# Performance work log

Measured on AMD Instinct MI355X. Metric: run time of the kernel, lower is better.

Reference implementation:

```python
import jax, jax.numpy as jnp
import numpy as np

# Dims: B INRs, N probe points, d_in=2 coords, hidden H, out D_OUT, proj P
B, N, D_IN, H, D_OUT, P = 128, 4096, 2, 128, 3, 128
W0_SIREN = 30.0  # SIREN frequency scale
LN_EPS = 1e-5


def setup_inputs() -> dict:
    key = jax.random.key(0)
    ks = jax.random.split(key, 12)
    sn = lambda k, shape, sc: (jax.random.normal(k, shape, dtype=jnp.float32) * sc)
    return {
        # per-sample SIREN params, torch layout: weight [b, in, out, 1], bias [b, out, 1]
        "w0": sn(ks[0], (B, D_IN, H, 1), 1.0 / D_IN),
        "w1": sn(ks[1], (B, H, H, 1), np.sqrt(6.0 / H) / W0_SIREN),
        "w2": sn(ks[2], (B, H, D_OUT, 1), np.sqrt(6.0 / H) / W0_SIREN),
        "b0": sn(ks[3], (B, H, 1), 0.1),
        "b1": sn(ks[4], (B, H, 1), 0.1),
        "b2": sn(ks[5], (B, D_OUT, 1), 0.1),
        # learned probe coordinates, initialized U[-1, 1) as in the module
        "inputs": jax.random.uniform(ks[6], (1, N, D_IN), dtype=jnp.float32, minval=-1.0, maxval=1.0),
        # projection (num_inputs -> proj_dim) + LayerNorm params, one per probed layer (4 total)
        "pw": sn(ks[7], (4, N, P), 1.0 / np.sqrt(N)),
        "pb": jnp.zeros((4, P), jnp.float32),
        "ln_g": jnp.ones((4, P), jnp.float32),
        "ln_b": jnp.zeros((4, P), jnp.float32),
    }


def _layernorm(x, g, b):
    m = jnp.mean(x, axis=-1, keepdims=True)
    v = jnp.mean(jnp.square(x - m), axis=-1, keepdims=True)
    return (x - m) * jax.lax.rsqrt(v + LN_EPS) * g + b


def reference(w0, w1, w2, b0, b1, b2, inputs, pw, pb, ln_g, ln_b):
    b = w0.shape[0]
    x = jnp.broadcast_to(inputs, (b,) + inputs.shape[1:])  # [b, n, d_in]

    def lin(h, W, bb):
        # per-sample linear: [b,n,i] @ [b,i,o] + [b,1,o]
        return jnp.einsum('bni,bio->bno', h, W[..., 0]) + bb[:, None, :, 0]

    h1 = jnp.sin(W0_SIREN * lin(x, w0, b0))   # [b, n, H]
    h2 = jnp.sin(W0_SIREN * lin(h1, w1, b1))  # [b, n, H]
    h3 = lin(h2, w2, b2)                      # [b, n, D_OUT] (last layer: no sine)
    feats = [x, h1, h2, h3]  # probe features per node layer (input coords + activations)

    outs = []
    for i, f in enumerate(feats):
        # permute to [b, dim_i, n], project n -> P, then LayerNorm over P
        z = jnp.einsum('bnd,np->bdp', f, pw[i]) + pb[i]
        outs.append(_layernorm(z, ln_g[i], ln_b[i]))
    return jnp.concatenate(outs, axis=1)  # [b, d_in + H + H + D_OUT, P]
```

## Files before the change

kernel.cpp:

```cpp
#include <hip/hip_runtime.h>


typedef unsigned short u16;
typedef __attribute__((ext_vector_type(8))) short short8;
typedef __attribute__((ext_vector_type(4))) short short4v;
typedef __attribute__((ext_vector_type(4))) float f32x4;
typedef __attribute__((ext_vector_type(4))) float float4v;

#define DEV __device__ __forceinline__
#define R30 4.774648292756860f

DEV float b2f(u16 h){ return __uint_as_float(((unsigned)h) << 16); }
DEV u16 f2b(float f){
  unsigned u = __float_as_uint(f);
  return (u16)((u + 0x7FFFu + ((u >> 16) & 1u)) >> 16);
}
DEV float sin_rev(float r){
  r = r - rintf(r);
#if __has_builtin(__builtin_amdgcn_sinf)
  return __builtin_amdgcn_sinf(r);
#else
  return __sinf(r * 6.283185307179586f);
#endif
}
template<int C> DEV float dpp_add(float x){
  int yi = __builtin_amdgcn_update_dpp(0, __float_as_int(x), C, 0xF, 0xF, true);
  return x + __int_as_float(yi);
}
DEV float sum16(float x){
  x = dpp_add<0x128>(x); x = dpp_add<0x124>(x);
  x = dpp_add<0x122>(x); x = dpp_add<0x121>(x);
  return x;
}

DEV int is_bf16_fmt(const void* lng){ return *(const unsigned*)lng == 0x3F803F80u; }
struct In {
  const float* f; const u16* h; int bf;
  DEV In(const void* p, int b_) : f((const float*)p), h((const u16*)p), bf(b_) {}
  DEV float at(size_t i) const { return bf ? b2f(h[i]) : f[i]; }
};

__global__ __launch_bounds__(256) void k_prep(const void* pwv, const void* inpv,
                                              const void* lngv,
                                              u16* __restrict__ pwT,
                                              float* __restrict__ xbuf){
  const int bf = is_bf16_fmt(lngv);
  const int t = threadIdx.x;
  if (blockIdx.x == 256){
    In inp(inpv, bf);
    for (int i = t; i < 8192; i += 256) xbuf[i] = inp.at(i);
    return;
  }
  In pw(pwv, bf);
  __shared__ u16 tile[64 * 129];
  const int layer = blockIdx.x >> 6;
  const int n0 = (blockIdx.x & 63) * 64;
  const size_t base = ((size_t)layer * 4096 + n0) * 128;
#pragma unroll
  for (int k = 0; k < 32; k++){
    int idx = k * 256 + t, n = idx >> 7, p = idx & 127;
    tile[n * 129 + p] = f2b(pw.at(base + (size_t)n * 128 + p));
  }
  __syncthreads();
  u16* dst = pwT + (size_t)layer * 128 * 4096 + n0;
#pragma unroll
  for (int k = 0; k < 32; k++){
    int idx = k * 256 + t, p = idx >> 6, n = idx & 63;
    dst[(size_t)p * 4096 + n] = tile[n * 129 + p];
  }
}

#define S_NK 136
#define S_T  40

template<bool PARTIAL>
__global__ __launch_bounds__(512, 2)
void k_main(const void* w0v, const void* w1v, const void* w2v,
            const void* b0v, const void* b1v, const void* b2v,
            const void* pbv, const void* lgv, const void* lbv,
            const u16* __restrict__ pwTg, const float* __restrict__ xbuf,
            float* __restrict__ outp, int TS){
  __shared__ __align__(16) u16 spw[4][128 * S_T];
  __shared__ __align__(16) u16 sh1nk[32 * S_NK];
  __shared__ __align__(16) u16 sh1T[128 * S_T];
  __shared__ __align__(16) u16 sh2T[128 * S_T];
  __shared__ __align__(16) u16 sxT[16 * S_T];
  __shared__ float sW2[512];
  __shared__ float sb2[4];
  __shared__ float sPB[512], sG[512], sBB[512];

  float* sP1 = (float*)sh1nk;
  float* sP2 = (float*)sh1T;
  float* sM  = (float*)sh2T;
  float* sI  = (float*)sh2T + 512;

  const int bf = is_bf16_fmt(lgv);
  In w0(w0v, bf), w1(w1v, bf), w2(w2v, bf), b0(b0v, bf), b1(b1v, bf),
     b2(b2v, bf), pb(pbv, bf), lg(lgv, bf), lb(lbv, bf);

  const int t = threadIdx.x;
  const int b = blockIdx.x & 127, sseg = blockIdx.x >> 7;
  const int lane = t & 63, wave = t >> 6, quad = lane >> 4, r16 = lane & 15;
  const int oo = wave * 16 + r16;

  if (t >= 256 && t < 384){
    int i = t - 256;
    sW2[i * 4 + 0] = w2.at(((size_t)b * 128 + i) * 3 + 0);
    sW2[i * 4 + 1] = w2.at(((size_t)b * 128 + i) * 3 + 1);
    sW2[i * 4 + 2] = w2.at(((size_t)b * 128 + i) * 3 + 2);
    sW2[i * 4 + 3] = 0.f;
  }
  if (t < 4) sb2[t] = (t < 3) ? b2.at(b * 3 + t) : 0.f;
  sPB[t] = pb.at(t); sG[t] = lg.at(t); sBB[t] = lb.at(t);
  for (int k = t; k < 16 * S_T; k += 512) sxT[k] = 0;

  const int p1n = t >> 4, p1hb = (t & 15) * 8;
  float w00[8], w01[8], b00[8];
#pragma unroll
  for (int j = 0; j < 8; j++){
    w00[j] = w0.at((size_t)b * 256 + p1hb + j) * R30;
    w01[j] = w0.at((size_t)b * 256 + 128 + p1hb + j) * R30;
    b00[j] = b0.at((size_t)b * 128 + p1hb + j) * R30;
  }
  const int p2h = t & 127, p2nb = (t >> 7) * 8;
  const float q00 = w0.at((size_t)b * 256 + p2h) * R30;
  const float q01 = w0.at((size_t)b * 256 + 128 + p2h) * R30;
  const float qb0 = b0.at((size_t)b * 128 + p2h) * R30;
  const float bias1r = b1.at((size_t)b * 128 + oo) * R30;

  short8 w1f[4];
#pragma unroll
  for (int ks = 0; ks < 4; ks++){
#pragma unroll
    for (int j = 0; j < 8; j++)
      w1f[ks][j] = (short)f2b(w1.at((size_t)b * 16384 +
                                    (size_t)(ks * 32 + quad * 8 + j) * 128 + oo));
  }
  short8 a1s = {0,0,0,0,0,0,0,0};
  if (r16 == 0){
#pragma unroll
    for (int j = 0; j < 8; j++) a1s[j] = (short)0x3F80;
  }

  const int pwrow = t >> 2, pwc = t & 3;
  const u16* pwsrc = pwTg + (size_t)pwrow * 4096 + pwc * 8;
  const int pwdofs = pwrow * S_T + pwc * 8;
  const int bofs = oo * S_T + quad * 8;

  const f32x4 zz = {0.f,0.f,0.f,0.f};
  f32x4 az1[8], az2[8], ay[8], az0 = zz, az3 = zz;
#pragma unroll
  for (int i = 0; i < 8; i++){ az1[i] = zz; az2[i] = zz; ay[i] = zz; }

  const int n0first = sseg * TS * 32;
  short8 pwv[4];
#pragma unroll
  for (int L = 0; L < 4; L++)
    pwv[L] = *(const short8*)(pwsrc + (size_t)L * 524288 + n0first);
  float2 xp1 = *(const float2*)(xbuf + (size_t)(n0first + p1n) * 2);

  __syncthreads();

  for (int nt = 0; nt < TS; nt++){
    const int n0 = (sseg * TS + nt) * 32;

    float4v xq[4];
#pragma unroll
    for (int q = 0; q < 4; q++)
      xq[q] = *(const float4v*)(xbuf + (size_t)(n0 + p2nb) * 2 + q * 4);
#pragma unroll
    for (int L = 0; L < 4; L++)
      *(short8*)&spw[L][pwdofs] = pwv[L];
    if ((t & 15) == 0){
      sxT[p1n] = f2b(xp1.x);
      sxT[S_T + p1n] = f2b(xp1.y);
    }
    {
      short8 v;
#pragma unroll
      for (int j = 0; j < 8; j++)
        v[j] = (short)f2b(sin_rev(fmaf(xp1.y, w01[j], fmaf(xp1.x, w00[j], b00[j]))));
      *(short8*)&sh1nk[p1n * S_NK + p1hb] = v;
    }
    {
      short8 v;
#pragma unroll
      for (int j = 0; j < 8; j++){
        float x0 = xq[j >> 1][(j & 1) * 2], x1 = xq[j >> 1][(j & 1) * 2 + 1];
        v[j] = (short)f2b(sin_rev(fmaf(x1, q01, fmaf(x0, q00, qb0))));
      }
      *(short8*)&sh1T[p2h * S_T + p2nb] = v;
    }
    __syncthreads();

    {
      const int nn = (nt + 1 < TS) ? nt + 1 : nt;
      const int n0n = (sseg * TS + nn) * 32;
      short8 pwn[4];
#pragma unroll
      for (int L = 0; L < 4; L++)
        pwn[L] = *(const short8*)(pwsrc + (size_t)L * 524288 + n0n);
      float2 xp1n = *(const float2*)(xbuf + (size_t)(n0n + p1n) * 2);

      f32x4 h0 = zz, h1a = zz;
#pragma unroll
      for (int ks = 0; ks < 4; ks++){
        h0  = __builtin_amdgcn_mfma_f32_16x16x32_bf16(
                *(short8*)&sh1nk[r16 * S_NK + ks * 32 + quad * 8], w1f[ks], h0, 0, 0, 0);
        h1a = __builtin_amdgcn_mfma_f32_16x16x32_bf16(
                *(short8*)&sh1nk[(16 + r16) * S_NK + ks * 32 + quad * 8], w1f[ks], h1a, 0, 0, 0);
      }
      az0 = __builtin_amdgcn_mfma_f32_16x16x32_bf16(
              *(short8*)&sxT[r16 * S_T + quad * 8], *(short8*)&spw[0][bofs], az0, 0, 0, 0);
#pragma unroll
      for (int mb = 0; mb < 8; mb++)
        az1[mb] = __builtin_amdgcn_mfma_f32_16x16x32_bf16(
                    *(short8*)&sh1T[(mb * 16 + r16) * S_T + quad * 8],
                    *(short8*)&spw[1][bofs], az1[mb], 0, 0, 0);
      az3 = __builtin_amdgcn_mfma_f32_16x16x32_bf16(a1s, *(short8*)&spw[3][bofs], az3, 0, 0, 0);
      {
        short4v v;
#pragma unroll
        for (int r = 0; r < 4; r++) v[r] = (short)f2b(sin_rev(fmaf(h0[r], R30, bias1r)));
        *(short4v*)&sh2T[oo * S_T + quad * 4] = v;
#pragma unroll
        for (int r = 0; r < 4; r++) v[r] = (short)f2b(sin_rev(fmaf(h1a[r], R30, bias1r)));
        *(short4v*)&sh2T[oo * S_T + 16 + quad * 4] = v;
      }
      __syncthreads();

#pragma unroll
      for (int mb = 0; mb < 8; mb++){
        short8 a = *(short8*)&sh2T[(mb * 16 + r16) * S_T + quad * 8];
        az2[mb] = __builtin_amdgcn_mfma_f32_16x16x32_bf16(a, *(short8*)&spw[2][bofs], az2[mb], 0, 0, 0);
        ay[mb]  = __builtin_amdgcn_mfma_f32_16x16x32_bf16(a, *(short8*)&spw[3][bofs], ay[mb], 0, 0, 0);
      }

#pragma unroll
      for (int L = 0; L < 4; L++) pwv[L] = pwn[L];
      xp1 = xp1n;
    }
    __syncthreads();
  }

  const int p = oo;
  float S3 = (quad == 0) ? az3[0] : 0.f;
  S3 += __shfl_xor(S3, 16, 64); S3 += __shfl_xor(S3, 32, 64);
  float z3v[3];
#pragma unroll
  for (int d = 0; d < 3; d++){
    float a = 0.f;
#pragma unroll
    for (int mb = 0; mb < 8; mb++)
#pragma unroll
      for (int r = 0; r < 4; r++)
        a = fmaf(sW2[(mb * 16 + quad * 4 + r) * 4 + d], ay[mb][r], a);
    a += __shfl_xor(a, 16, 64); a += __shfl_xor(a, 32, 64);
    z3v[d] = a + sb2[d] * S3;
  }

  if (PARTIAL){
    float* zp = outp + ((size_t)(sseg * 128 + b)) * 261 * 128;
    if (quad == 0){
#pragma unroll
      for (int r = 0; r < 2; r++) zp[(size_t)r * 128 + p] = az0[r];
#pragma unroll
      for (int d = 0; d < 3; d++) zp[(size_t)(258 + d) * 128 + p] = z3v[d];
    }
#pragma unroll
    for (int mb = 0; mb < 8; mb++)
#pragma unroll
      for (int r = 0; r < 4; r++){
        int drow = mb * 16 + quad * 4 + r;
        zp[(size_t)(2 + drow) * 128 + p]   = az1[mb][r];
        zp[(size_t)(130 + drow) * 128 + p] = az2[mb][r];
      }
    return;
  }

  const float pb0v = sPB[p],       pb1v = sPB[128 + p];
  const float pb2v = sPB[256 + p], pb3v = sPB[384 + p];

  auto rowsum = [&](float v, int row, bool wr){
    float s1 = sum16(v), s2 = sum16(v * v);
    if (wr && r16 == 0){ sP1[row * 8 + wave] = s1; sP2[row * 8 + wave] = s2; }
  };
#pragma unroll
  for (int r = 0; r < 2; r++) rowsum(az0[r] + pb0v, r, quad == 0);
#pragma unroll
  for (int mb = 0; mb < 8; mb++)
#pragma unroll
    for (int r = 0; r < 4; r++)
      rowsum(az1[mb][r] + pb1v, 2 + mb * 16 + quad * 4 + r, true);
#pragma unroll
  for (int mb = 0; mb < 8; mb++)
#pragma unroll
    for (int r = 0; r < 4; r++)
      rowsum(az2[mb][r] + pb2v, 130 + mb * 16 + quad * 4 + r, true);
#pragma unroll
  for (int d = 0; d < 3; d++) rowsum(z3v[d] + pb3v, 258 + d, quad == 0);
  __syncthreads();

  if (t < 261){
    float s1 = 0.f, s2 = 0.f;
#pragma unroll
    for (int w = 0; w < 8; w++){ s1 += sP1[t * 8 + w]; s2 += sP2[t * 8 + w]; }
    float m = s1 * (1.f / 128.f);
    float var = fmaf(-m, m, s2 * (1.f / 128.f));
    sM[t] = m;
    sI[t] = rsqrtf(fmaxf(var, 0.f) + 1e-5f);
  }
  __syncthreads();

  const size_t ob = (size_t)b * 261 * 128;
  auto emit = [&](float v, int row, int grp){
    outp[ob + (size_t)row * 128 + p] =
      (v - sM[row]) * sI[row] * sG[grp * 128 + p] + sBB[grp * 128 + p];
  };
  if (quad == 0){
#pragma unroll
    for (int r = 0; r < 2; r++) emit(az0[r] + pb0v, r, 0);
#pragma unroll
    for (int d = 0; d < 3; d++) emit(z3v[d] + pb3v, 258 + d, 3);
  }
#pragma unroll
  for (int mb = 0; mb < 8; mb++)
#pragma unroll
    for (int r = 0; r < 4; r++)
      emit(az1[mb][r] + pb1v, 2 + mb * 16 + quad * 4 + r, 1);
#pragma unroll
  for (int mb = 0; mb < 8; mb++)
#pragma unroll
    for (int r = 0; r < 4; r++)
      emit(az2[mb][r] + pb2v, 130 + mb * 16 + quad * 4 + r, 2);
}

__global__ __launch_bounds__(256)
void k_ln(const float* __restrict__ zp, const void* pbv, const void* lgv,
          const void* lbv, float* __restrict__ out, int split){
  const int bf = is_bf16_fmt(lgv);
  In pb(pbv, bf), lg(lgv, bf), lb(lbv, bf);
  const int lane = threadIdx.x & 63;
  const int row = blockIdx.x * 4 + (threadIdx.x >> 6);
  const int b = row / 261, d = row % 261;
  const int grp = (d < 2) ? 0 : (d < 130) ? 1 : (d < 258) ? 2 : 3;
  const int p0 = lane * 2;
  float v0 = pb.at(grp * 128 + p0), v1 = pb.at(grp * 128 + p0 + 1);
  for (int s2 = 0; s2 < split; s2++){
    const float* zr = zp + ((size_t)(s2 * 128 + b) * 261 + d) * 128;
    v0 += zr[p0]; v1 += zr[p0 + 1];
  }
  float s1 = v0 + v1, s2s = v0 * v0 + v1 * v1;
#pragma unroll
  for (int o = 1; o < 64; o <<= 1){
    s1 += __shfl_xor(s1, o, 64);
    s2s += __shfl_xor(s2s, o, 64);
  }
  float m = s1 * (1.f / 128.f);
  float var = fmaf(-m, m, s2s * (1.f / 128.f));
  float inv = rsqrtf(fmaxf(var, 0.f) + 1e-5f);
  float2 o2;
  o2.x = (v0 - m) * inv * lg.at(grp * 128 + p0)     + lb.at(grp * 128 + p0);
  o2.y = (v1 - m) * inv * lg.at(grp * 128 + p0 + 1) + lb.at(grp * 128 + p0 + 1);
  *(float2*)(out + (size_t)row * 128 + p0) = o2;
}

extern "C" void kernel_launch(void* const* d_in, const int* in_sizes, int n_in,
                              void* d_out, int out_size, void* d_ws, size_t ws_size,
                              hipStream_t stream){
  const void* w0  = d_in[0];
  const void* w1  = d_in[1];
  const void* w2  = d_in[2];
  const void* b0  = d_in[3];
  const void* b1  = d_in[4];
  const void* b2  = d_in[5];
  const void* inp = d_in[6];
  const void* pw  = d_in[7];
  const void* pb  = d_in[8];
  const void* lng = d_in[9];
  const void* lnb = d_in[10];
  float* out = (float*)d_out;

  u16* pwT    = (u16*)d_ws;
  float* xbuf = (float*)((char*)d_ws + (size_t)4 * 128 * 4096 * 2);
  const size_t zoff = (size_t)4 * 128 * 4096 * 2 + 8192 * 4;
  float* zp = (float*)((char*)d_ws + zoff);
  const size_t seg = (size_t)128 * 261 * 128 * 4;

  int split = 1;
  if (ws_size >= zoff + 4 * seg) split = 4;
  else if (ws_size >= zoff + 2 * seg) split = 2;

  k_prep<<<257, 256, 0, stream>>>(pw, inp, lng, pwT, xbuf);
  if (split > 1){
    k_main<true><<<128 * split, 512, 0, stream>>>(w0, w1, w2, b0, b1, b2,
        pb, lng, lnb, pwT, xbuf, zp, 128 / split);
    k_ln<<<(128 * 261) / 4, 256, 0, stream>>>(zp, pb, lng, lnb, out, split);
  } else {
    k_main<false><<<128, 512, 0, stream>>>(w0, w1, w2, b0, b1, b2,
        pb, lng, lnb, pwT, xbuf, out, 128);
  }
}
```

Before: 256.5 us.

## Double-buffer activation tiles, load projection weights directly to registers, cap split at two

Drops the shared-memory staging of the projection weights. Each lane now loads its pw fragment straight from global memory into registers for the MFMA B operand. The activation tiles (h1, h2, x) are double-buffered so one barrier per iteration can be removed, and bf16 packing uses the hardware packed-convert instruction. The N-split is capped at 2 (256 blocks) instead of 4. Together these aim to cut LDS traffic and barrier count. The trade-offs are a global-load latency that is no longer prefetched a tile ahead, and less parallelism from the smaller split.

Result: slower. 292.4 us (+14.0%).

```diff
diff --git a/kernel.cpp b/kernel.cpp
--- a/kernel.cpp
+++ b/kernel.cpp
@@ -14,6 +14,21 @@
 DEV u16 f2b(float f){
   unsigned u = __float_as_uint(f);
   return (u16)((u + 0x7FFFu + ((u >> 16) & 1u)) >> 16);
+}
+DEV unsigned pkcvt(float a, float b){
+#if __has_builtin(__builtin_amdgcn_cvt_pk_bf16_f32)
+  typedef __attribute__((ext_vector_type(2))) __bf16 bf16x2;
+  bf16x2 v = __builtin_amdgcn_cvt_pk_bf16_f32(a, b);
+  return *(unsigned*)&v;
+#else
+  return (unsigned)f2b(a) | (((unsigned)f2b(b)) << 16);
+#endif
+}
+DEV short8 pack8(const float* f){
+  union { unsigned u[4]; short8 s; } r;
+#pragma unroll
+  for (int j = 0; j < 4; j++) r.u[j] = pkcvt(f[2*j], f[2*j+1]);
+  return r.s;
 }
 DEV float sin_rev(float r){
   r = r - rintf(r);
@@ -80,19 +95,18 @@
             const void* pbv, const void* lgv, const void* lbv,
             const u16* __restrict__ pwTg, const float* __restrict__ xbuf,
             float* __restrict__ outp, int TS){
-  __shared__ __align__(16) u16 spw[4][128 * S_T];
-  __shared__ __align__(16) u16 sh1nk[32 * S_NK];
-  __shared__ __align__(16) u16 sh1T[128 * S_T];
-  __shared__ __align__(16) u16 sh2T[128 * S_T];
-  __shared__ __align__(16) u16 sxT[16 * S_T];
+  __shared__ __align__(16) u16 sh1nk[2][32 * S_NK];
+  __shared__ __align__(16) u16 sh1T[2][128 * S_T];
+  __shared__ __align__(16) u16 sh2T[2][128 * S_T];
+  __shared__ __align__(16) u16 sxT[2][16 * S_T];
   __shared__ float sW2[512];
   __shared__ float sb2[4];
   __shared__ float sPB[512], sG[512], sBB[512];
 
-  float* sP1 = (float*)sh1nk;
-  float* sP2 = (float*)sh1T;
-  float* sM  = (float*)sh2T;
-  float* sI  = (float*)sh2T + 512;
+  float* sP1 = (float*)&sh1nk[0][0];
+  float* sP2 = (float*)&sh1T[0][0];
+  float* sM  = (float*)&sh2T[0][0];
+  float* sI  = (float*)&sh2T[0][0] + 512;
 
   const int bf = is_bf16_fmt(lgv);
   In w0(w0v, bf), w1(w1v, bf), w2(w2v, bf), b0(b0v, bf), b1(b1v, bf),
@@ -112,7 +126,7 @@
   }
   if (t < 4) sb2[t] = (t < 3) ? b2.at(b * 3 + t) : 0.f;
   sPB[t] = pb.at(t); sG[t] = lg.at(t); sBB[t] = lb.at(t);
-  for (int k = t; k < 16 * S_T; k += 512) sxT[k] = 0;
+  for (int k = t; k < 2 * 16 * S_T; k += 512) sxT[0][k] = 0;
 
   const int p1n = t >> 4, p1hb = (t & 15) * 8;
   float w00[8], w01[8], b00[8];
@@ -142,105 +156,86 @@
     for (int j = 0; j < 8; j++) a1s[j] = (short)0x3F80;
   }
 
-  const int pwrow = t >> 2, pwc = t & 3;
-  const u16* pwsrc = pwTg + (size_t)pwrow * 4096 + pwc * 8;
-  const int pwdofs = pwrow * S_T + pwc * 8;
-  const int bofs = oo * S_T + quad * 8;
+  const u16* pwbase = pwTg + (size_t)oo * 4096 + quad * 8;
 
   const f32x4 zz = {0.f,0.f,0.f,0.f};
   f32x4 az1[8], az2[8], ay[8], az0 = zz, az3 = zz;
 #pragma unroll
   for (int i = 0; i < 8; i++){ az1[i] = zz; az2[i] = zz; ay[i] = zz; }
 
-  const int n0first = sseg * TS * 32;
-  short8 pwv[4];
-#pragma unroll
-  for (int L = 0; L < 4; L++)
-    pwv[L] = *(const short8*)(pwsrc + (size_t)L * 524288 + n0first);
-  float2 xp1 = *(const float2*)(xbuf + (size_t)(n0first + p1n) * 2);
-
   __syncthreads();
 
   for (int nt = 0; nt < TS; nt++){
+    const int buf = nt & 1;
     const int n0 = (sseg * TS + nt) * 32;
 
-    float4v xq[4];
-#pragma unroll
-    for (int q = 0; q < 4; q++)
-      xq[q] = *(const float4v*)(xbuf + (size_t)(n0 + p2nb) * 2 + q * 4);
+    short8 pwf[4];
 #pragma unroll
     for (int L = 0; L < 4; L++)
-      *(short8*)&spw[L][pwdofs] = pwv[L];
-    if ((t & 15) == 0){
-      sxT[p1n] = f2b(xp1.x);
-      sxT[S_T + p1n] = f2b(xp1.y);
+      pwf[L] = *(const short8*)(pwbase + (size_t)L * 524288 + n0);
+    if (t < 64){
+      int n = t >> 1, c = t & 1;
+      sxT[buf][c * S_T + n] = f2b(xbuf[(size_t)(n0 + n) * 2 + c]);
     }
     {
-      short8 v;
+      float2 xv = *(const float2*)(xbuf + (size_t)(n0 + p1n) * 2);
+      float vv[8];
 #pragma unroll
       for (int j = 0; j < 8; j++)
-        v[j] = (short)f2b(sin_rev(fmaf(xp1.y, w01[j], fmaf(xp1.x, w00[j], b00[j]))));
-      *(short8*)&sh1nk[p1n * S_NK + p1hb] = v;
+        vv[j] = sin_rev(fmaf(xv.y, w01[j], fmaf(xv.x, w00[j], b00[j])));
+      *(short8*)&sh1nk[buf][p1n * S_NK + p1hb] = pack8(vv);
     }
     {
-      short8 v;
+      float4v xq[4];
+#pragma unroll
+      for (int q = 0; q < 4; q++)
+        xq[q] = *(const float4v*)(xbuf + (size_t)(n0 + p2nb) * 2 + q * 4);
+      float vv[8];
 #pragma unroll
       for (int j = 0; j < 8; j++){
         float x0 = xq[j >> 1][(j & 1) * 2], x1 = xq[j >> 1][(j & 1) * 2 + 1];
-        v[j] = (short)f2b(sin_rev(fmaf(x1, q01, fmaf(x0, q00, qb0))));
+        vv[j] = sin_rev(fmaf(x1, q01, fmaf(x0, q00, qb0)));
       }
-      *(short8*)&sh1T[p2h * S_T + p2nb] = v;
+      *(short8*)&sh1T[buf][p2h * S_T + p2nb] = pack8(vv);
     }
     __syncthreads();
 
+    f32x4 h0 = zz, h1a = zz;
+#pragma unroll
+    for (int ks = 0; ks < 4; ks++){
+      h0  = __builtin_amdgcn_mfma_f32_16x16x32_bf16(
+              *(short8*)&sh1nk[buf][r16 * S_NK + ks * 32 + quad * 8], w1f[ks], h0, 0, 0, 0);
+      h1a = __builtin_amdgcn_mfma_f32_16x16x32_bf16(
+              *(short8*)&sh1nk[buf][(16 + r16) * S_NK + ks * 32 + quad * 8], w1f[ks], h1a, 0, 0, 0);
+    }
+    az0 = __builtin_amdgcn_mfma_f32_16x16x32_bf16(
+            *(short8*)&sxT[buf][r16 * S_T + quad * 8], pwf[0], az0, 0, 0, 0);
+#pragma unroll
+    for (int mb = 0; mb < 8; mb++)
+      az1[mb] = __builtin_amdgcn_mfma_f32_16x16x32_bf16(
+                  *(short8*)&sh1T[buf][(mb * 16 + r16) * S_T + quad * 8],
+                  pwf[1], az1[mb], 0, 0, 0);
+    az3 = __builtin_amdgcn_mfma_f32_16x16x32_bf16(a1s, pwf[3], az3, 0, 0, 0);
     {
-      const int nn = (nt + 1 < TS) ? nt + 1 : nt;
-      const int n0n = (sseg * TS + nn) * 32;
-      short8 pwn[4];
-#pragma unroll
-      for (int L = 0; L < 4; L++)
-        pwn[L] = *(const short8*)(pwsrc + (size_t)L * 524288 + n0n);
-      float2 xp1n = *(const float2*)(xbuf + (size_t)(n0n + p1n) * 2);
-
-      f32x4 h0 = zz, h1a = zz;
-#pragma unroll
-      for (int ks = 0; ks < 4; ks++){
-        h0  = __builtin_amdgcn_mfma_f32_16x16x32_bf16(
-                *(short8*)&sh1nk[r16 * S_NK + ks * 32 + quad * 8], w1f[ks], h0, 0, 0, 0);
-        h1a = __builtin_amdgcn_mfma_f32_16x16x32_bf16(
-                *(short8*)&sh1nk[(16 + r16) * S_NK + ks * 32 + quad * 8], w1f[ks], h1a, 0, 0, 0);
-      }
-      az0 = __builtin_amdgcn_mfma_f32_16x16x32_bf16(
-              *(short8*)&sxT[r16 * S_T + quad * 8], *(short8*)&spw[0][bofs], az0, 0, 0, 0);
-#pragma unroll
-      for (int mb = 0; mb < 8; mb++)
-        az1[mb] = __builtin_amdgcn_mfma_f32_16x16x32_bf16(
-                    *(short8*)&sh1T[(mb * 16 + r16) * S_T + quad * 8],
-                    *(short8*)&spw[1][bofs], az1[mb], 0, 0, 0);
-      az3 = __builtin_amdgcn_mfma_f32_16x16x32_bf16(a1s, *(short8*)&spw[3][bofs], az3, 0, 0, 0);
-      {
-        short4v v;
-#pragma unroll
-        for (int r = 0; r < 4; r++) v[r] = (short)f2b(sin_rev(fmaf(h0[r], R30, bias1r)));
-        *(short4v*)&sh2T[oo * S_T + quad * 4] = v;
-#pragma unroll
-        for (int r = 0; r < 4; r++) v[r] = (short)f2b(sin_rev(fmaf(h1a[r], R30, bias1r)));
-        *(short4v*)&sh2T[oo * S_T + 16 + quad * 4] = v;
-      }
-      __syncthreads();
-
-#pragma unroll
-      for (int mb = 0; mb < 8; mb++){
-        short8 a = *(short8*)&sh2T[(mb * 16 + r16) * S_T + quad * 8];
-        az2[mb] = __builtin_amdgcn_mfma_f32_16x16x32_bf16(a, *(short8*)&spw[2][bofs], az2[mb], 0, 0, 0);
-        ay[mb]  = __builtin_amdgcn_mfma_f32_16x16x32_bf16(a, *(short8*)&spw[3][bofs], ay[mb], 0, 0, 0);
-      }
-
-#pragma unroll
-      for (int L = 0; L < 4; L++) pwv[L] = pwn[L];
-      xp1 = xp1n;
+      unsigned* d0 = (unsigned*)&sh2T[buf][oo * S_T + quad * 4];
+      d0[0] = pkcvt(sin_rev(fmaf(h0[0], R30, bias1r)),
+                    sin_rev(fmaf(h0[1], R30, bias1r)));
+      d0[1] = pkcvt(sin_rev(fmaf(h0[2], R30, bias1r)),
+                    sin_rev(fmaf(h0[3], R30, bias1r)));
+      unsigned* d1 = (unsigned*)&sh2T[buf][oo * S_T + 16 + quad * 4];
+      d1[0] = pkcvt(sin_rev(fmaf(h1a[0], R30, bias1r)),
+                    sin_rev(fmaf(h1a[1], R30, bias1r)));
+      d1[1] = pkcvt(sin_rev(fmaf(h1a[2], R30, bias1r)),
+                    sin_rev(fmaf(h1a[3], R30, bias1r)));
     }
     __syncthreads();
+
+#pragma unroll
+    for (int mb = 0; mb < 8; mb++){
+      short8 a = *(short8*)&sh2T[buf][(mb * 16 + r16) * S_T + quad * 8];
+      az2[mb] = __builtin_amdgcn_mfma_f32_16x16x32_bf16(a, pwf[2], az2[mb], 0, 0, 0);
+      ay[mb]  = __builtin_amdgcn_mfma_f32_16x16x32_bf16(a, pwf[3], ay[mb], 0, 0, 0);
+    }
   }
 
   const int p = oo;
@@ -278,6 +273,7 @@
     return;
   }
 
+  __syncthreads();
   const float pb0v = sPB[p],       pb1v = sPB[128 + p];
   const float pb2v = sPB[256 + p], pb3v = sPB[384 + p];
 
@@ -387,15 +383,13 @@
   float* zp = (float*)((char*)d_ws + zoff);
   const size_t seg = (size_t)128 * 261 * 128 * 4;
 
-  int split = 1;
-  if (ws_size >= zoff + 4 * seg) split = 4;
-  else if (ws_size >= zoff + 2 * seg) split = 2;
+  const int split = (ws_size >= zoff + 2 * seg) ? 2 : 1;
 
   k_prep<<<257, 256, 0, stream>>>(pw, inp, lng, pwT, xbuf);
-  if (split > 1){
-    k_main<true><<<128 * split, 512, 0, stream>>>(w0, w1, w2, b0, b1, b2,
-        pb, lng, lnb, pwT, xbuf, zp, 128 / split);
-    k_ln<<<(128 * 261) / 4, 256, 0, stream>>>(zp, pb, lng, lnb, out, split);
+  if (split == 2){
+    k_main<true><<<256, 512, 0, stream>>>(w0, w1, w2, b0, b1, b2,
+        pb, lng, lnb, pwT, xbuf, zp, 64);
+    k_ln<<<(128 * 261) / 4, 256, 0, stream>>>(zp, pb, lng, lnb, out, 2);
   } else {
     k_main<false><<<128, 512, 0, stream>>>(w0, w1, w2, b0, b1, b2,
         pb, lng, lnb, pwT, xbuf, out, 128);
```
